# Performance work log

Hardware: AMD Instinct MI355X
Metric: run time of the kernel (lower is better)

Reference implementation:

```python
import itertools
import jax, jax.numpy as jnp
import numpy as np

N = 400000
CIN, COUT = 32, 64
K, STRIDE, PAD, DIL = 3, 2, 1, 1
SPATIAL = (200, 200, 16)
PRUNING_RATIO = 0.5

def _out_spatial():
    return tuple((s + 2 * PAD - DIL * (K - 1) - 1) // STRIDE + 1 for s in SPATIAL)


def setup_inputs() -> dict:
    key = jax.random.key(0)
    kf, kc0, kc1, kc2, kc3, km, kw = jax.random.split(key, 7)
    features = jax.random.normal(kf, (N, CIN), dtype=jnp.float32)
    b = jax.random.randint(kc0, (N,), 0, 2, dtype=jnp.int32)
    z = jax.random.randint(kc1, (N,), 0, SPATIAL[0], dtype=jnp.int32)
    y = jax.random.randint(kc2, (N,), 0, SPATIAL[1], dtype=jnp.int32)
    x = jax.random.randint(kc3, (N,), 0, SPATIAL[2], dtype=jnp.int32)
    coors = jnp.stack([b, z, y, x], axis=1)  # [N,4] = (batch, d0, d1, d2)
    mask = jax.random.uniform(km, (N,), dtype=jnp.float32)
    weight = jax.random.normal(kw, (K, K, K, CIN, COUT), dtype=jnp.float32) * 0.05
    return {"features": features, "coors": coors, "mask": mask, "weight": weight, "batch_size": 2}


def _sprs_conv(features, coors, mask, weight, batch_size):
    out_sp = _out_spatial()  # (100, 100, 8)
    num_out = batch_size * out_sp[0] * out_sp[1] * out_sp[2]
    n = features.shape[0]
    # rank-based pruning: keep top (1 - pruning_ratio) points as 'important'
    thr = jnp.sort(mask)[int(n * PRUNING_RATIO)]
    important = (mask >= thr)  # [N] bool

    b = coors[:, 0]
    pos = coors[:, 1:4]  # [N,3]
    out_sp_arr = jnp.array(out_sp, dtype=pos.dtype)

    # accumulators; slot num_out is a dump for invalid indices
    acc = jnp.zeros((num_out + 1, COUT), dtype=features.dtype)
    imp_cnt = jnp.zeros((num_out + 1,), dtype=jnp.int32)

    for off in itertools.product(range(K), repeat=3):
        off_arr = jnp.array(off, dtype=pos.dtype)
        num = pos + PAD - DIL * off_arr  # [N,3]
        oc = num // STRIDE
        valid = jnp.all(num % STRIDE == 0, axis=-1) & jnp.all(oc >= 0, axis=-1) & jnp.all(oc < out_sp_arr, axis=-1)
        lin = ((b * out_sp[0] + oc[:, 0]) * out_sp[1] + oc[:, 1]) * out_sp[2] + oc[:, 2]
        idx = jnp.where(valid, lin, num_out)
        vals = features @ weight[off[0], off[1], off[2]]  # [N,Cout] gather-GEMM
        acc = acc.at[idx].add(vals)  # scatter
        imp_cnt = imp_cnt.at[idx].add((important & valid).astype(jnp.int32))

    keep = (imp_cnt[:num_out] > 0)  # output positions reached by >=1 important point
    return acc[:num_out] * keep[:, None]


def reference(features, coors, mask, weight, batch_size):
    return _sprs_conv(features, coors, mask, weight, batch_size)
```

## Files before the change

### kernel.cpp

```cpp
#include <hip/hip_runtime.h>

#define CIN 32
#define COUT 64
#define OD0 100
#define OD1 100
#define OD2 8
#define IZ 200
#define IY 200
#define IX 16
#define NTAP 27
#define NCELLS (2 * IZ * IY * IX)
#define TOY 4
#define TOX 8
#define NROW 27
#define NCELL_R (NROW * 16)
#define CAPB 384


__global__ void hist0_fused_kernel(const float* __restrict__ mask, const int* __restrict__ coors,
                                   const float* __restrict__ W, int n,
                                   int* __restrict__ hist, int* __restrict__ S,
                                   float* __restrict__ Wt) {
    __shared__ int h[256];
    h[threadIdx.x] = 0;
    __syncthreads();
    for (int i = blockIdx.x * blockDim.x + threadIdx.x; i < n; i += gridDim.x * blockDim.x) {
        unsigned bits = __float_as_uint(mask[i]);
        atomicAdd(&h[bits >> 24], 1);
        const int4 c = ((const int4*)coors)[i];
        atomicAdd(&S[((c.x * IZ + c.y) * IY + c.z) * IX + c.w], 1);
    }
    for (int i = blockIdx.x * blockDim.x + threadIdx.x; i < NTAP * CIN * COUT;
         i += gridDim.x * blockDim.x) {
        int cout = i % COUT;
        int rest = i / COUT;
        int cin = rest % CIN;
        int tap = rest / CIN;
        Wt[((size_t)tap * COUT + cout) * CIN + cin] = W[i];
    }
    __syncthreads();
    int v = h[threadIdx.x];
    if (v) atomicAdd(&hist[threadIdx.x], v);
}


__global__ void hist8_kernel(const float* __restrict__ mask, int n, int level,
                             const int* __restrict__ state, int* __restrict__ hist) {
    __shared__ int h[256];
    h[threadIdx.x] = 0;
    __syncthreads();
    unsigned pfx = (unsigned)state[0];
    int sh = 24 - 8 * level;
    for (int i = blockIdx.x * blockDim.x + threadIdx.x; i < n; i += gridDim.x * blockDim.x) {
        unsigned bits = __float_as_uint(mask[i]);
        if ((bits >> (sh + 8)) == pfx)
            atomicAdd(&h[(bits >> sh) & 0xFF], 1);
    }
    __syncthreads();
    int v = h[threadIdx.x];
    if (v) atomicAdd(&hist[threadIdx.x], v);
}

__global__ void select8_kernel(const int* __restrict__ hist, int* __restrict__ state,
                               int level, int rankConst) {
    __shared__ int sc[256];
    sc[threadIdx.x] = hist[threadIdx.x];
    __syncthreads();
    if (threadIdx.x == 0) {
        int rank = level ? state[1] : rankConst;
        unsigned pfx = level ? (unsigned)state[0] : 0u;
        int c = 0;
        for (int j = 0; j < 256; j++) {
            int hv = sc[j];
            if (rank < c + hv) {
                state[0] = (int)((pfx << 8) | (unsigned)j);
                state[1] = rank - c;
                break;
            }
            c += hv;
        }
    }
}


__global__ void scan_l0_kernel(int* __restrict__ S, int* __restrict__ partials) {
    __shared__ int ts[256];
    int tid = threadIdx.x;
    int4 v = ((int4*)S)[blockIdx.x * 256 + tid];
    int s1 = v.x + v.y, s2 = s1 + v.z, s3 = s2 + v.w;
    ts[tid] = s3;
    __syncthreads();
    for (int off = 1; off < 256; off <<= 1) {
        int t = (tid >= off) ? ts[tid - off] : 0;
        __syncthreads();
        ts[tid] += t;
        __syncthreads();
    }
    int excl = ts[tid] - s3;
    int4 o;
    o.x = excl; o.y = excl + v.x; o.z = excl + s1; o.w = excl + s2;
    ((int4*)S)[blockIdx.x * 256 + tid] = o;
    if (tid == 255) partials[blockIdx.x] = ts[255];
}

__global__ void scan_l1_kernel(int* __restrict__ partials, int nP) {
    __shared__ int sums[256];
    int tid = threadIdx.x;
    int per = (nP + 255) / 256;
    int lo = tid * per, hi = lo + per;
    if (hi > nP) hi = nP;
    int s = 0;
    for (int j = lo; j < hi; j++) s += partials[j];
    sums[tid] = s;
    __syncthreads();
    for (int off = 1; off < 256; off <<= 1) {
        int t = (tid >= off) ? sums[tid - off] : 0;
        __syncthreads();
        sums[tid] += t;
        __syncthreads();
    }
    int run = sums[tid] - s;
    for (int j = lo; j < hi; j++) { int v = partials[j]; partials[j] = run; run += v; }
}

__global__ void scan_l2_kernel(int* __restrict__ S, const int* __restrict__ partials) {
    int add = partials[blockIdx.x];
    if (add == 0) return;
    int4 v = ((int4*)S)[blockIdx.x * 256 + threadIdx.x];
    v.x += add; v.y += add; v.z += add; v.w += add;
    ((int4*)S)[blockIdx.x * 256 + threadIdx.x] = v;
}

__global__ void scatter_points_kernel(const int* __restrict__ coors, const float* __restrict__ mask,
                                      const int* __restrict__ state, int n,
                                      int* __restrict__ S, int* __restrict__ entries) {
    int i = blockIdx.x * blockDim.x + threadIdx.x;
    if (i >= n) return;
    const int4 c = ((const int4*)coors)[i];
    int cell = ((c.x * IZ + c.y) * IY + c.z) * IX + c.w;
    float thr = __uint_as_float((unsigned)state[0]);
    int imp = (mask[i] >= thr) ? 1 : 0;
    int pos = atomicAdd(&S[cell], 1);
    entries[pos] = (i << 1) | imp;
}


__global__ void __launch_bounds__(256)
conv_kernel(const float* __restrict__ feat, const float* __restrict__ Wt,
            const int* __restrict__ S, const int* __restrict__ entries,
            float* __restrict__ out) {
    __shared__ float accS[TOY * TOX][COUT];
    __shared__ int   keepS[TOY * TOX];
    __shared__ int   sLds[NROW][17];
    __shared__ unsigned work[6][CAPB];
    __shared__ int   cnt[6];
    __shared__ int   notDone;

    int tid = threadIdx.x;
    int w = tid >> 6;
    int lane = tid & 63;

    int tile = blockIdx.x;
    int oyT = (tile % (OD1 / TOY)) * TOY;
    int rest = tile / (OD1 / TOY);
    int oz = rest % OD0;
    int bb = rest / OD0;

    {
        float4 z = make_float4(0.f, 0.f, 0.f, 0.f);
        float4* a4 = (float4*)&accS[0][0];
        a4[tid] = z;
        a4[tid + 256] = z;
        if (tid < TOY * TOX) keepS[tid] = 0;
    }

    for (int idx = tid; idx < NROW * 17; idx += 256) {
        int row = idx / 17, j = idx % 17;
        int plane = row / 9, pyL = row % 9;
        int pz = 2 * oz - 1 + plane;
        int py = 2 * oyT - 1 + pyL;
        int v = 0;
        if (pz >= 0 && py >= 0) {
            int cellFlat = ((bb * IZ + pz) * IY + py) * IX + (j - 1);
            if (cellFlat >= 0) v = S[cellFlat];
        }
        sLds[row][j] = v;
    }
    __syncthreads();

    int myCl[2]; int nMy = 0;
    for (int cl = tid; cl < NCELL_R; cl += 256) myCl[nMy++] = cl;
    int ci = 0;
    int pi = -1;

    for (;;) {
        if (tid < 6) cnt[tid] = 0;
        if (tid == 0) notDone = 0;
        __syncthreads();

        while (ci < nMy) {
            int cl = myCl[ci];
            int row = cl >> 4, px = cl & 15;
            int rs = (pi < 0) ? sLds[row][px] : pi;
            int re = sLds[row][px + 1];
            int plane = row / 9, pyL = row % 9;
            int bin = plane * 2 + (pyL & 1);
            bool blocked = false;
            for (int i = rs; i < re; i++) {
                int pos = atomicAdd(&cnt[bin], 1);
                if (pos >= CAPB) { pi = i; blocked = true; break; }
                int e = entries[i];
                work[bin][pos] = ((unsigned)(e >> 1) << 9) | (unsigned)((e & 1) << 8)
                               | (unsigned)(pyL << 4) | (unsigned)px;
            }
            if (blocked) break;
            ci++; pi = -1;
        }
        if (ci < nMy) notDone = 1;
        __syncthreads();

        for (int t = w; t < NTAP; t += 4) {
            int o0 = t / 9, r9 = t % 9, o1 = r9 / 3, o2 = r9 % 3;
            int bin = o0 * 2 + (o1 & 1);
            int nb = cnt[bin];
            if (nb > CAPB) nb = CAPB;
            if (nb == 0) continue;

            const float4* wp = (const float4*)(Wt + ((size_t)t * COUT + lane) * CIN);
            float4 w0 = wp[0], w1 = wp[1], w2 = wp[2], w3 = wp[3];
            float4 w4 = wp[4], w5 = wp[5], w6 = wp[6], w7 = wp[7];

            int pcl = -1;
            float4 f0, f1, f2, f3, f4, f5, f6, f7;

            for (int j = 0; j < nb; j++) {
                unsigned e = work[bin][j];
                int pyL = (int)((e >> 4) & 15u);
                int px  = (int)(e & 15u);
                int yy = (pyL - o1) >> 1;
                if ((unsigned)yy >= (unsigned)TOY) continue;
                int dx = px + 1 - o2;
                if (dx & 1) continue;
                int ox = dx >> 1;
                if ((unsigned)ox >= (unsigned)TOX) continue;

                int pid = (int)(e >> 9);
                const float4* fp = (const float4*)(feat + (size_t)pid * CIN);
                float4 n0 = fp[0], n1 = fp[1], n2 = fp[2], n3 = fp[3];
                float4 n4 = fp[4], n5 = fp[5], n6 = fp[6], n7 = fp[7];

                if (pcl >= 0) {
                    float a0 = 0.f, a1 = 0.f, a2 = 0.f, a3 = 0.f;
                    a0 = fmaf(f0.x, w0.x, a0); a0 = fmaf(f0.y, w0.y, a0);
                    a0 = fmaf(f0.z, w0.z, a0); a0 = fmaf(f0.w, w0.w, a0);
                    a1 = fmaf(f1.x, w1.x, a1); a1 = fmaf(f1.y, w1.y, a1);
                    a1 = fmaf(f1.z, w1.z, a1); a1 = fmaf(f1.w, w1.w, a1);
                    a2 = fmaf(f2.x, w2.x, a2); a2 = fmaf(f2.y, w2.y, a2);
                    a2 = fmaf(f2.z, w2.z, a2); a2 = fmaf(f2.w, w2.w, a2);
                    a3 = fmaf(f3.x, w3.x, a3); a3 = fmaf(f3.y, w3.y, a3);
                    a3 = fmaf(f3.z, w3.z, a3); a3 = fmaf(f3.w, w3.w, a3);
                    a0 = fmaf(f4.x, w4.x, a0); a0 = fmaf(f4.y, w4.y, a0);
                    a0 = fmaf(f4.z, w4.z, a0); a0 = fmaf(f4.w, w4.w, a0);
                    a1 = fmaf(f5.x, w5.x, a1); a1 = fmaf(f5.y, w5.y, a1);
                    a1 = fmaf(f5.z, w5.z, a1); a1 = fmaf(f5.w, w5.w, a1);
                    a2 = fmaf(f6.x, w6.x, a2); a2 = fmaf(f6.y, w6.y, a2);
                    a2 = fmaf(f6.z, w6.z, a2); a2 = fmaf(f6.w, w6.w, a2);
                    a3 = fmaf(f7.x, w7.x, a3); a3 = fmaf(f7.y, w7.y, a3);
                    a3 = fmaf(f7.z, w7.z, a3); a3 = fmaf(f7.w, w7.w, a3);
                    atomicAdd(&accS[pcl][lane], (a0 + a1) + (a2 + a3));
                }

                f0 = n0; f1 = n1; f2 = n2; f3 = n3;
                f4 = n4; f5 = n5; f6 = n6; f7 = n7;
                pcl = yy * TOX + ox;
                if (lane == 0 && (e & 0x100u)) keepS[pcl] = 1;
            }

            if (pcl >= 0) {
                float a0 = 0.f, a1 = 0.f, a2 = 0.f, a3 = 0.f;
                a0 = fmaf(f0.x, w0.x, a0); a0 = fmaf(f0.y, w0.y, a0);
                a0 = fmaf(f0.z, w0.z, a0); a0 = fmaf(f0.w, w0.w, a0);
                a1 = fmaf(f1.x, w1.x, a1); a1 = fmaf(f1.y, w1.y, a1);
                a1 = fmaf(f1.z, w1.z, a1); a1 = fmaf(f1.w, w1.w, a1);
                a2 = fmaf(f2.x, w2.x, a2); a2 = fmaf(f2.y, w2.y, a2);
                a2 = fmaf(f2.z, w2.z, a2); a2 = fmaf(f2.w, w2.w, a2);
                a3 = fmaf(f3.x, w3.x, a3); a3 = fmaf(f3.y, w3.y, a3);
                a3 = fmaf(f3.z, w3.z, a3); a3 = fmaf(f3.w, w3.w, a3);
                a0 = fmaf(f4.x, w4.x, a0); a0 = fmaf(f4.y, w4.y, a0);
                a0 = fmaf(f4.z, w4.z, a0); a0 = fmaf(f4.w, w4.w, a0);
                a1 = fmaf(f5.x, w5.x, a1); a1 = fmaf(f5.y, w5.y, a1);
                a1 = fmaf(f5.z, w5.z, a1); a1 = fmaf(f5.w, w5.w, a1);
                a2 = fmaf(f6.x, w6.x, a2); a2 = fmaf(f6.y, w6.y, a2);
                a2 = fmaf(f6.z, w6.z, a2); a2 = fmaf(f6.w, w6.w, a2);
                a3 = fmaf(f7.x, w7.x, a3); a3 = fmaf(f7.y, w7.y, a3);
                a3 = fmaf(f7.z, w7.z, a3); a3 = fmaf(f7.w, w7.w, a3);
                atomicAdd(&accS[pcl][lane], (a0 + a1) + (a2 + a3));
            }
        }
        __syncthreads();
        if (!notDone) break;
    }

#pragma unroll
    for (int k = 0; k < 8; k++) {
        int cl = w * 8 + k;
        int oy = oyT + (cl >> 3);
        int ox = cl & 7;
        size_t cellG = (((size_t)bb * OD0 + oz) * OD1 + oy) * OD2 + ox;
        out[cellG * COUT + lane] = keepS[cl] ? accS[cl][lane] : 0.f;
    }
}


__global__ void hist0_simple_kernel(const float* __restrict__ mask, int n, int* __restrict__ hist) {
    __shared__ int h[256];
    h[threadIdx.x] = 0;
    __syncthreads();
    for (int i = blockIdx.x * blockDim.x + threadIdx.x; i < n; i += gridDim.x * blockDim.x) {
        unsigned bits = __float_as_uint(mask[i]);
        atomicAdd(&h[bits >> 24], 1);
    }
    __syncthreads();
    int v = h[threadIdx.x];
    if (v) atomicAdd(&hist[threadIdx.x], v);
}

__global__ void __launch_bounds__(256)
scatter_kernel(const float* __restrict__ feat, const int* __restrict__ coors,
               const float* __restrict__ mask, const float* __restrict__ W,
               const int* __restrict__ state, float* __restrict__ out,
               int* __restrict__ keep, int n) {
    int gid = blockIdx.x * blockDim.x + threadIdx.x;
    int wave = gid >> 6;
    int lane = threadIdx.x & 63;
    if (wave >= n) return;

    const int4 c4 = ((const int4*)coors)[wave];
    int bb = c4.x, pz = c4.y, py = c4.z, px = c4.w;

    float thr = __uint_as_float((unsigned)state[0]);
    bool imp = mask[wave] >= thr;

    int oz[2], ozo[2], nz = 0;
    int oy[2], oyo[2], ny = 0;
    int ox[2], oxo[2], nx = 0;
#pragma unroll
    for (int o = 0; o < 3; o++) {
        int num = pz + 1 - o;
        if (num >= 0 && !(num & 1) && (num >> 1) < OD0) { oz[nz] = num >> 1; ozo[nz] = o; nz++; }
        num = py + 1 - o;
        if (num >= 0 && !(num & 1) && (num >> 1) < OD1) { oy[ny] = num >> 1; oyo[ny] = o; ny++; }
        num = px + 1 - o;
        if (num >= 0 && !(num & 1) && (num >> 1) < OD2) { ox[nx] = num >> 1; oxo[nx] = o; nx++; }
    }

    float f[CIN];
    const float4* fp = (const float4*)(feat + (size_t)wave * CIN);
#pragma unroll
    for (int j = 0; j < CIN / 4; j++) {
        float4 v = fp[j];
        f[4 * j + 0] = v.x; f[4 * j + 1] = v.y; f[4 * j + 2] = v.z; f[4 * j + 3] = v.w;
    }

    for (int a = 0; a < nz; a++)
        for (int b = 0; b < ny; b++)
            for (int c = 0; c < nx; c++) {
                int woff = ((ozo[a] * 3 + oyo[b]) * 3 + oxo[c]) * (CIN * COUT);
                const float* wcol = W + woff + lane;
                float acc = 0.f;
#pragma unroll
                for (int k = 0; k < CIN; k++) acc = fmaf(f[k], wcol[k * COUT], acc);
                int lin = ((bb * OD0 + oz[a]) * OD1 + oy[b]) * OD2 + ox[c];
                atomicAdd(out + (size_t)lin * COUT + lane, acc);
                if (imp && lane == 0) keep[lin] = 1;
            }
}

__global__ void finalize_kernel(float* __restrict__ out, const int* __restrict__ keep, int numOut) {
    int t = blockIdx.x * blockDim.x + threadIdx.x;
    if (t >= numOut * (COUT / 4)) return;
    int o = t >> 4;
    if (!keep[o]) ((float4*)out)[t] = make_float4(0.f, 0.f, 0.f, 0.f);
}


extern "C" void kernel_launch(void* const* d_in, const int* in_sizes, int n_in,
                              void* d_out, int out_size, void* d_ws, size_t ws_size,
                              hipStream_t stream) {
    const float* feat  = (const float*)d_in[0];
    const int*   coors = (const int*)d_in[1];
    const float* mask  = (const float*)d_in[2];
    const float* W     = (const float*)d_in[3];

    int n = in_sizes[2];
    int numOut = out_size / COUT;
    int rank = (int)(n * 0.5);

    const int blk = 256;
    int gN = (n + blk - 1) / blk;

    char* ws = (char*)d_ws;

    size_t offHist    = 0;
    size_t offState   = 4 * 256 * 4;
    size_t offS       = offState + 64;
    size_t offPart    = offS + (size_t)NCELLS * 4;
    size_t offEntries = offPart + 1280 * 4;
    size_t offWt      = offEntries + (size_t)n * 4;
    size_t need       = offWt + (size_t)NTAP * CIN * COUT * 4;

    int* hist  = (int*)(ws + offHist);
    int* state = (int*)(ws + offState);

    if (ws_size >= need) {
        int*   S       = (int*)(ws + offS);
        int*   part    = (int*)(ws + offPart);
        int*   entries = (int*)(ws + offEntries);
        float* Wt      = (float*)(ws + offWt);

        hipMemsetAsync(ws, 0, offS + (size_t)NCELLS * 4, stream);

        hist0_fused_kernel<<<256, blk, 0, stream>>>(mask, coors, W, n, hist, S, Wt);
        select8_kernel<<<1, 256, 0, stream>>>(hist, state, 0, rank);
        for (int lvl = 1; lvl < 4; lvl++) {
            hist8_kernel<<<256, blk, 0, stream>>>(mask, n, lvl, state, hist + lvl * 256);
            select8_kernel<<<1, 256, 0, stream>>>(hist + lvl * 256, state, lvl, rank);
        }

        int nBlocksScan = NCELLS / 1024;
        scan_l0_kernel<<<nBlocksScan, 256, 0, stream>>>(S, part);
        scan_l1_kernel<<<1, 256, 0, stream>>>(part, nBlocksScan);
        scan_l2_kernel<<<nBlocksScan, 256, 0, stream>>>(S, part);
        scatter_points_kernel<<<gN, blk, 0, stream>>>(coors, mask, state, n, S, entries);

        int nTiles = numOut / (TOY * TOX);
        conv_kernel<<<nTiles, 256, 0, stream>>>(feat, Wt, S, entries, (float*)d_out);
    } else {
        int* keep = (int*)(ws + offS);
        hipMemsetAsync(d_out, 0, (size_t)out_size * sizeof(float), stream);
        hipMemsetAsync(ws, 0, offS + (size_t)numOut * 4, stream);

        hist0_simple_kernel<<<256, blk, 0, stream>>>(mask, n, hist);
        select8_kernel<<<1, 256, 0, stream>>>(hist, state, 0, rank);
        for (int lvl = 1; lvl < 4; lvl++) {
            hist8_kernel<<<256, blk, 0, stream>>>(mask, n, lvl, state, hist + lvl * 256);
            select8_kernel<<<1, 256, 0, stream>>>(hist + lvl * 256, state, lvl, rank);
        }

        long long threads = (long long)n * 64;
        int gScatter = (int)((threads + blk - 1) / blk);
        scatter_kernel<<<gScatter, blk, 0, stream>>>(feat, coors, mask, W, state,
                                                     (float*)d_out, keep, n);

        int fin = numOut * (COUT / 4);
        finalize_kernel<<<(fin + blk - 1) / blk, blk, 0, stream>>>((float*)d_out, keep, numOut);
    }
}
```

Before: 733.6 us.

## Stage gathered point features in LDS once per round for reuse across taps

The conv kernel now assigns each gathered point a slot, loads its 32-float feature row into shared memory once per work round, and has every tap read features from LDS instead of reloading them from global memory per tap. This removes up to eight redundant global gathers of the same point (one per tap sharing a bin) and the software-pipelined register prefetch. In exchange it adds an extra barrier and cooperative load phase per round, uses more LDS (which may lower occupancy), and caps rounds at 176 points, which may force more rounds.

```diff
diff --git a/kernel.cpp b/kernel.cpp
--- a/kernel.cpp
+++ b/kernel.cpp
@@ -14,7 +14,8 @@
 #define TOX 8
 #define NROW 27
 #define NCELL_R (NROW * 16)
-#define CAPB 384
+#define CAPB 256
+#define CAPF 176
 
 
 __global__ void hist0_fused_kernel(const float* __restrict__ mask, const int* __restrict__ coors,
@@ -150,10 +151,13 @@
             const int* __restrict__ S, const int* __restrict__ entries,
             float* __restrict__ out) {
     __shared__ float accS[TOY * TOX][COUT];
+    __shared__ float featL[CAPF][CIN];
     __shared__ int   keepS[TOY * TOX];
     __shared__ int   sLds[NROW][17];
     __shared__ unsigned work[6][CAPB];
+    __shared__ int   slotPid[CAPF];
     __shared__ int   cnt[6];
+    __shared__ int   nPts;
     __shared__ int   notDone;
 
     int tid = threadIdx.x;
@@ -195,7 +199,7 @@
 
     for (;;) {
         if (tid < 6) cnt[tid] = 0;
-        if (tid == 0) notDone = 0;
+        if (tid == 0) { nPts = 0; notDone = 0; }
         __syncthreads();
 
         while (ci < nMy) {
@@ -209,14 +213,36 @@
             for (int i = rs; i < re; i++) {
                 int pos = atomicAdd(&cnt[bin], 1);
                 if (pos >= CAPB) { pi = i; blocked = true; break; }
+                int slot = atomicAdd(&nPts, 1);
+                if (slot >= CAPF) {
+                    work[bin][pos] = 0xFFFFFFFFu;
+                    pi = i; blocked = true; break;
+                }
                 int e = entries[i];
-                work[bin][pos] = ((unsigned)(e >> 1) << 9) | (unsigned)((e & 1) << 8)
+                slotPid[slot] = e >> 1;
+                work[bin][pos] = ((unsigned)slot << 9) | (unsigned)((e & 1) << 8)
                                | (unsigned)(pyL << 4) | (unsigned)px;
             }
             if (blocked) break;
             ci++; pi = -1;
         }
         if (ci < nMy) notDone = 1;
+        __syncthreads();
+        int more = notDone;
+
+        {
+            int total = nPts;
+            if (total > CAPF) total = CAPF;
+            int col = lane & 7;
+            for (int s8 = w * 8; s8 < total; s8 += 32) {
+                int s = s8 + (lane >> 3);
+                if (s < total) {
+                    int pid = slotPid[s];
+                    ((float4*)&featL[s][0])[col] =
+                        ((const float4*)(feat + (size_t)pid * CIN))[col];
+                }
+            }
+        }
         __syncthreads();
 
         for (int t = w; t < NTAP; t += 4) {
@@ -230,11 +256,9 @@
             float4 w0 = wp[0], w1 = wp[1], w2 = wp[2], w3 = wp[3];
             float4 w4 = wp[4], w5 = wp[5], w6 = wp[6], w7 = wp[7];
 
-            int pcl = -1;
-            float4 f0, f1, f2, f3, f4, f5, f6, f7;
-
             for (int j = 0; j < nb; j++) {
                 unsigned e = work[bin][j];
+                if (e == 0xFFFFFFFFu) continue;
                 int pyL = (int)((e >> 4) & 15u);
                 int px  = (int)(e & 15u);
                 int yy = (pyL - o1) >> 1;
@@ -244,39 +268,9 @@
                 int ox = dx >> 1;
                 if ((unsigned)ox >= (unsigned)TOX) continue;
 
-                int pid = (int)(e >> 9);
-                const float4* fp = (const float4*)(feat + (size_t)pid * CIN);
-                float4 n0 = fp[0], n1 = fp[1], n2 = fp[2], n3 = fp[3];
-                float4 n4 = fp[4], n5 = fp[5], n6 = fp[6], n7 = fp[7];
-
-                if (pcl >= 0) {
-                    float a0 = 0.f, a1 = 0.f, a2 = 0.f, a3 = 0.f;
-                    a0 = fmaf(f0.x, w0.x, a0); a0 = fmaf(f0.y, w0.y, a0);
-                    a0 = fmaf(f0.z, w0.z, a0); a0 = fmaf(f0.w, w0.w, a0);
-                    a1 = fmaf(f1.x, w1.x, a1); a1 = fmaf(f1.y, w1.y, a1);
-                    a1 = fmaf(f1.z, w1.z, a1); a1 = fmaf(f1.w, w1.w, a1);
-                    a2 = fmaf(f2.x, w2.x, a2); a2 = fmaf(f2.y, w2.y, a2);
-                    a2 = fmaf(f2.z, w2.z, a2); a2 = fmaf(f2.w, w2.w, a2);
-                    a3 = fmaf(f3.x, w3.x, a3); a3 = fmaf(f3.y, w3.y, a3);
-                    a3 = fmaf(f3.z, w3.z, a3); a3 = fmaf(f3.w, w3.w, a3);
-                    a0 = fmaf(f4.x, w4.x, a0); a0 = fmaf(f4.y, w4.y, a0);
-                    a0 = fmaf(f4.z, w4.z, a0); a0 = fmaf(f4.w, w4.w, a0);
-                    a1 = fmaf(f5.x, w5.x, a1); a1 = fmaf(f5.y, w5.y, a1);
-                    a1 = fmaf(f5.z, w5.z, a1); a1 = fmaf(f5.w, w5.w, a1);
-                    a2 = fmaf(f6.x, w6.x, a2); a2 = fmaf(f6.y, w6.y, a2);
-                    a2 = fmaf(f6.z, w6.z, a2); a2 = fmaf(f6.w, w6.w, a2);
-                    a3 = fmaf(f7.x, w7.x, a3); a3 = fmaf(f7.y, w7.y, a3);
-                    a3 = fmaf(f7.z, w7.z, a3); a3 = fmaf(f7.w, w7.w, a3);
-                    atomicAdd(&accS[pcl][lane], (a0 + a1) + (a2 + a3));
-                }
-
-                f0 = n0; f1 = n1; f2 = n2; f3 = n3;
-                f4 = n4; f5 = n5; f6 = n6; f7 = n7;
-                pcl = yy * TOX + ox;
-                if (lane == 0 && (e & 0x100u)) keepS[pcl] = 1;
-            }
-
-            if (pcl >= 0) {
+                const float4* fl = (const float4*)&featL[e >> 9][0];
+                float4 f0 = fl[0], f1 = fl[1], f2 = fl[2], f3 = fl[3];
+                float4 f4 = fl[4], f5 = fl[5], f6 = fl[6], f7 = fl[7];
                 float a0 = 0.f, a1 = 0.f, a2 = 0.f, a3 = 0.f;
                 a0 = fmaf(f0.x, w0.x, a0); a0 = fmaf(f0.y, w0.y, a0);
                 a0 = fmaf(f0.z, w0.z, a0); a0 = fmaf(f0.w, w0.w, a0);
@@ -294,11 +288,14 @@
                 a2 = fmaf(f6.z, w6.z, a2); a2 = fmaf(f6.w, w6.w, a2);
                 a3 = fmaf(f7.x, w7.x, a3); a3 = fmaf(f7.y, w7.y, a3);
                 a3 = fmaf(f7.z, w7.z, a3); a3 = fmaf(f7.w, w7.w, a3);
-                atomicAdd(&accS[pcl][lane], (a0 + a1) + (a2 + a3));
+
+                int cl = yy * TOX + ox;
+                atomicAdd(&accS[cl][lane], (a0 + a1) + (a2 + a3));
+                if (lane == 0 && (e & 0x100u)) keepS[cl] = 1;
             }
         }
         __syncthreads();
-        if (!notDone) break;
+        if (!more) break;
     }
 
 #pragma unroll
```

New measurement: 775.5 us. 1.06x slower.

## Fuse radix-select and scan stages using last-block-done atomics to cut launches

Applied to the files above, without the earlier changes.

Replaces the four-level histogram/select kernel chain with two histogram kernels that finish selection in the last block to arrive, a compaction pass that collects candidates matching the 16-bit prefix, and a single-block final selection over that small set. It also merges scan level 1 into scan level 0 through the same last-block pattern. The goal is fewer kernel launches and fewer full passes over the mask, trading them for global atomics, fences and reuse of the entries buffer as scratch.

```diff
diff --git a/kernel.cpp b/kernel.cpp
--- a/kernel.cpp
+++ b/kernel.cpp
@@ -16,21 +16,28 @@
 #define NCELL_R (NROW * 16)
 #define CAPB 384
 
-
-__global__ void hist0_fused_kernel(const float* __restrict__ mask, const int* __restrict__ coors,
-                                   const float* __restrict__ W, int n,
-                                   int* __restrict__ hist, int* __restrict__ S,
-                                   float* __restrict__ Wt) {
+#define ALOAD(p)     __hip_atomic_load((p), __ATOMIC_RELAXED, __HIP_MEMORY_SCOPE_AGENT)
+#define ASTORE(p, v) __hip_atomic_store((p), (v), __ATOMIC_RELAXED, __HIP_MEMORY_SCOPE_AGENT)
+#define ADONE(p)     __hip_atomic_fetch_add((p), 1, __ATOMIC_ACQ_REL, __HIP_MEMORY_SCOPE_AGENT)
+
+
+
+__global__ void histA_kernel(const float* __restrict__ mask, const int* __restrict__ coors,
+                             const float* __restrict__ W, int n, int rank,
+                             int* __restrict__ hist, int* __restrict__ state,
+                             int* __restrict__ S, float* __restrict__ Wt) {
     __shared__ int h[256];
-    h[threadIdx.x] = 0;
-    __syncthreads();
-    for (int i = blockIdx.x * blockDim.x + threadIdx.x; i < n; i += gridDim.x * blockDim.x) {
+    __shared__ int islast;
+    int tid = threadIdx.x;
+    h[tid] = 0;
+    __syncthreads();
+    for (int i = blockIdx.x * blockDim.x + tid; i < n; i += gridDim.x * blockDim.x) {
         unsigned bits = __float_as_uint(mask[i]);
         atomicAdd(&h[bits >> 24], 1);
         const int4 c = ((const int4*)coors)[i];
         atomicAdd(&S[((c.x * IZ + c.y) * IY + c.z) * IX + c.w], 1);
     }
-    for (int i = blockIdx.x * blockDim.x + threadIdx.x; i < NTAP * CIN * COUT;
+    for (int i = blockIdx.x * blockDim.x + tid; i < NTAP * CIN * COUT;
          i += gridDim.x * blockDim.x) {
         int cout = i % COUT;
         int rest = i / COUT;
@@ -39,42 +46,56 @@
         Wt[((size_t)tap * COUT + cout) * CIN + cin] = W[i];
     }
     __syncthreads();
-    int v = h[threadIdx.x];
-    if (v) atomicAdd(&hist[threadIdx.x], v);
-}
-
-
-__global__ void hist8_kernel(const float* __restrict__ mask, int n, int level,
-                             const int* __restrict__ state, int* __restrict__ hist) {
-    __shared__ int h[256];
-    h[threadIdx.x] = 0;
-    __syncthreads();
-    unsigned pfx = (unsigned)state[0];
-    int sh = 24 - 8 * level;
-    for (int i = blockIdx.x * blockDim.x + threadIdx.x; i < n; i += gridDim.x * blockDim.x) {
-        unsigned bits = __float_as_uint(mask[i]);
-        if ((bits >> (sh + 8)) == pfx)
-            atomicAdd(&h[(bits >> sh) & 0xFF], 1);
-    }
-    __syncthreads();
-    int v = h[threadIdx.x];
-    if (v) atomicAdd(&hist[threadIdx.x], v);
-}
-
-__global__ void select8_kernel(const int* __restrict__ hist, int* __restrict__ state,
-                               int level, int rankConst) {
-    __shared__ int sc[256];
-    sc[threadIdx.x] = hist[threadIdx.x];
-    __syncthreads();
-    if (threadIdx.x == 0) {
-        int rank = level ? state[1] : rankConst;
-        unsigned pfx = level ? (unsigned)state[0] : 0u;
+    if (h[tid]) atomicAdd(&hist[tid], h[tid]);
+    __threadfence();
+    __syncthreads();
+    if (tid == 0) islast = (ADONE(&state[4]) == (int)gridDim.x - 1);
+    __syncthreads();
+    if (!islast) return;
+    __threadfence();
+    h[tid] = ALOAD(&hist[tid]);
+    __syncthreads();
+    if (tid == 0) {
         int c = 0;
         for (int j = 0; j < 256; j++) {
-            int hv = sc[j];
-            if (rank < c + hv) {
-                state[0] = (int)((pfx << 8) | (unsigned)j);
-                state[1] = rank - c;
+            int hv = h[j];
+            if (rank < c + hv) { ASTORE(&state[0], j); ASTORE(&state[1], rank - c); break; }
+            c += hv;
+        }
+    }
+}
+
+
+__global__ void histB_kernel(const float* __restrict__ mask, int n,
+                             int* __restrict__ hist, int* __restrict__ state) {
+    __shared__ int h[256];
+    __shared__ int islast;
+    int tid = threadIdx.x;
+    unsigned pfx = (unsigned)state[0];
+    h[tid] = 0;
+    __syncthreads();
+    for (int i = blockIdx.x * blockDim.x + tid; i < n; i += gridDim.x * blockDim.x) {
+        unsigned bits = __float_as_uint(mask[i]);
+        if ((bits >> 24) == pfx) atomicAdd(&h[(bits >> 16) & 0xFF], 1);
+    }
+    __syncthreads();
+    if (h[tid]) atomicAdd(&hist[tid], h[tid]);
+    __threadfence();
+    __syncthreads();
+    if (tid == 0) islast = (ADONE(&state[5]) == (int)gridDim.x - 1);
+    __syncthreads();
+    if (!islast) return;
+    __threadfence();
+    h[tid] = ALOAD(&hist[tid]);
+    __syncthreads();
+    if (tid == 0) {
+        int rnk = state[1];
+        int c = 0;
+        for (int j = 0; j < 256; j++) {
+            int hv = h[j];
+            if (rnk < c + hv) {
+                ASTORE(&state[0], (int)((pfx << 8) | (unsigned)j));
+                ASTORE(&state[1], rnk - c);
                 break;
             }
             c += hv;
@@ -83,8 +104,67 @@
 }
 
 
-__global__ void scan_l0_kernel(int* __restrict__ S, int* __restrict__ partials) {
+__global__ void collect_kernel(const float* __restrict__ mask, int n,
+                               int* __restrict__ state, unsigned* __restrict__ scratch) {
+    int i = blockIdx.x * blockDim.x + threadIdx.x;
+    if (i >= n) return;
+    unsigned bits = __float_as_uint(mask[i]);
+    if ((int)(bits >> 16) == state[0]) {
+        int pos = atomicAdd(&state[6], 1);
+        scratch[pos] = bits;
+    }
+}
+
+
+__global__ void __launch_bounds__(1024)
+final_sel_kernel(const unsigned* __restrict__ scratch, int* __restrict__ state) {
+    __shared__ int h[256];
+    __shared__ int selb, srnk;
+    int tid = threadIdx.x;
+    int cnt = state[6];
+    unsigned pfx16 = (unsigned)state[0];
+    int rnk = state[1];
+    if (tid < 256) h[tid] = 0;
+    __syncthreads();
+    for (int i = tid; i < cnt; i += 1024)
+        atomicAdd(&h[(scratch[i] >> 8) & 0xFF], 1);
+    __syncthreads();
+    if (tid == 0) {
+        int c = 0;
+        for (int j = 0; j < 256; j++) {
+            int hv = h[j];
+            if (rnk < c + hv) { selb = j; srnk = rnk - c; break; }
+            c += hv;
+        }
+    }
+    __syncthreads();
+    int b2 = selb;
+    if (tid < 256) h[tid] = 0;
+    __syncthreads();
+    for (int i = tid; i < cnt; i += 1024) {
+        unsigned bits = scratch[i];
+        if ((int)((bits >> 8) & 0xFFu) == b2) atomicAdd(&h[bits & 0xFF], 1);
+    }
+    __syncthreads();
+    if (tid == 0) {
+        int r2 = srnk;
+        int c = 0;
+        for (int j = 0; j < 256; j++) {
+            int hv = h[j];
+            if (r2 < c + hv) {
+                state[0] = (int)((pfx16 << 16) | ((unsigned)b2 << 8) | (unsigned)j);
+                break;
+            }
+            c += hv;
+        }
+    }
+}
+
+
+__global__ void scan_l0f_kernel(int* __restrict__ S, int* __restrict__ partials,
+                                int* __restrict__ state, int nChunks) {
     __shared__ int ts[256];
+    __shared__ int islast;
     int tid = threadIdx.x;
     int4 v = ((int4*)S)[blockIdx.x * 256 + tid];
     int s1 = v.x + v.y, s2 = s1 + v.z, s3 = s2 + v.w;
@@ -100,27 +180,32 @@
     int4 o;
     o.x = excl; o.y = excl + v.x; o.z = excl + s1; o.w = excl + s2;
     ((int4*)S)[blockIdx.x * 256 + tid] = o;
-    if (tid == 255) partials[blockIdx.x] = ts[255];
-}
-
-__global__ void scan_l1_kernel(int* __restrict__ partials, int nP) {
-    __shared__ int sums[256];
-    int tid = threadIdx.x;
-    int per = (nP + 255) / 256;
+    if (tid == 255) ASTORE(&partials[blockIdx.x], ts[255]);
+    __threadfence();
+    __syncthreads();
+    if (tid == 0) islast = (ADONE(&state[7]) == (int)gridDim.x - 1);
+    __syncthreads();
+    if (!islast) return;
+    __threadfence();
+    int per = (nChunks + 255) / 256;
     int lo = tid * per, hi = lo + per;
-    if (hi > nP) hi = nP;
+    if (hi > nChunks) hi = nChunks;
     int s = 0;
-    for (int j = lo; j < hi; j++) s += partials[j];
-    sums[tid] = s;
+    for (int j = lo; j < hi; j++) s += ALOAD(&partials[j]);
+    ts[tid] = s;
     __syncthreads();
     for (int off = 1; off < 256; off <<= 1) {
-        int t = (tid >= off) ? sums[tid - off] : 0;
-        __syncthreads();
-        sums[tid] += t;
-        __syncthreads();
-    }
-    int run = sums[tid] - s;
-    for (int j = lo; j < hi; j++) { int v = partials[j]; partials[j] = run; run += v; }
+        int t = (tid >= off) ? ts[tid - off] : 0;
+        __syncthreads();
+        ts[tid] += t;
+        __syncthreads();
+    }
+    int run = ts[tid] - s;
+    for (int j = lo; j < hi; j++) {
+        int v2 = ALOAD(&partials[j]);
+        ASTORE(&partials[j], run);
+        run += v2;
+    }
 }
 
 __global__ void scan_l2_kernel(int* __restrict__ S, const int* __restrict__ partials) {
@@ -218,6 +303,7 @@
         }
         if (ci < nMy) notDone = 1;
         __syncthreads();
+        int more = notDone;
 
         for (int t = w; t < NTAP; t += 4) {
             int o0 = t / 9, r9 = t % 9, o1 = r9 / 3, o2 = r9 % 3;
@@ -298,7 +384,7 @@
             }
         }
         __syncthreads();
-        if (!notDone) break;
+        if (!more) break;
     }
 
 #pragma unroll
@@ -323,6 +409,44 @@
     __syncthreads();
     int v = h[threadIdx.x];
     if (v) atomicAdd(&hist[threadIdx.x], v);
+}
+
+__global__ void hist8_kernel(const float* __restrict__ mask, int n, int level,
+                             const int* __restrict__ state, int* __restrict__ hist) {
+    __shared__ int h[256];
+    h[threadIdx.x] = 0;
+    __syncthreads();
+    unsigned pfx = (unsigned)state[0];
+    int sh = 24 - 8 * level;
+    for (int i = blockIdx.x * blockDim.x + threadIdx.x; i < n; i += gridDim.x * blockDim.x) {
+        unsigned bits = __float_as_uint(mask[i]);
+        if ((bits >> (sh + 8)) == pfx)
+            atomicAdd(&h[(bits >> sh) & 0xFF], 1);
+    }
+    __syncthreads();
+    int v = h[threadIdx.x];
+    if (v) atomicAdd(&hist[threadIdx.x], v);
+}
+
+__global__ void select8_kernel(const int* __restrict__ hist, int* __restrict__ state,
+                               int level, int rankConst) {
+    __shared__ int sc[256];
+    sc[threadIdx.x] = hist[threadIdx.x];
+    __syncthreads();
+    if (threadIdx.x == 0) {
+        int rank = level ? state[1] : rankConst;
+        unsigned pfx = level ? (unsigned)state[0] : 0u;
+        int c = 0;
+        for (int j = 0; j < 256; j++) {
+            int hv = sc[j];
+            if (rank < c + hv) {
+                state[0] = (int)((pfx << 8) | (unsigned)j);
+                state[1] = rank - c;
+                break;
+            }
+            c += hv;
+        }
+    }
 }
 
 __global__ void __launch_bounds__(256)
@@ -420,16 +544,13 @@
 
         hipMemsetAsync(ws, 0, offS + (size_t)NCELLS * 4, stream);
 
-        hist0_fused_kernel<<<256, blk, 0, stream>>>(mask, coors, W, n, hist, S, Wt);
-        select8_kernel<<<1, 256, 0, stream>>>(hist, state, 0, rank);
-        for (int lvl = 1; lvl < 4; lvl++) {
-            hist8_kernel<<<256, blk, 0, stream>>>(mask, n, lvl, state, hist + lvl * 256);
-            select8_kernel<<<1, 256, 0, stream>>>(hist + lvl * 256, state, lvl, rank);
-        }
+        histA_kernel<<<256, blk, 0, stream>>>(mask, coors, W, n, rank, hist, state, S, Wt);
+        histB_kernel<<<256, blk, 0, stream>>>(mask, n, hist + 256, state);
+        collect_kernel<<<gN, blk, 0, stream>>>(mask, n, state, (unsigned*)entries);
+        final_sel_kernel<<<1, 1024, 0, stream>>>((const unsigned*)entries, state);
 
         int nBlocksScan = NCELLS / 1024;
-        scan_l0_kernel<<<nBlocksScan, 256, 0, stream>>>(S, part);
-        scan_l1_kernel<<<1, 256, 0, stream>>>(part, nBlocksScan);
+        scan_l0f_kernel<<<nBlocksScan, 256, 0, stream>>>(S, part, state, nBlocksScan);
         scan_l2_kernel<<<nBlocksScan, 256, 0, stream>>>(S, part);
         scatter_points_kernel<<<gN, blk, 0, stream>>>(coors, mask, state, n, S, entries);
 
```

Measured after the change: 902.7 us. 23.0% more time.
